# Performance work log

Hardware: AMD Instinct MI355X
Metric: run time of the kernel (lower is better)

Reference implementation:

```python
import jax, jax.numpy as jnp
import numpy as np

NUM_EMBEDDINGS = 512
EMBEDDING_DIM = 64
COMMITMENT_COST = 0.25


def setup_inputs() -> dict:
    key = jax.random.key(0)
    k1, k2 = jax.random.split(key)
    x = jax.random.normal(k1, (32, 64, 64, 64), dtype=jnp.float32)  # [B, C=D, H, W]
    # torch init: uniform(-1/K, 1/K)
    w = jax.random.uniform(k2, (NUM_EMBEDDINGS, EMBEDDING_DIM), dtype=jnp.float32,
                           minval=-1.0 / NUM_EMBEDDINGS, maxval=1.0 / NUM_EMBEDDINGS)
    return {"x": x, "w": w}


def reference(x, w):
    # [B, C, H, W] -> [B, H, W, C]
    xt = jnp.transpose(x, (0, 2, 3, 1))
    flat = xt.reshape(-1, EMBEDDING_DIM)  # [N, D]
    # squared L2 distances to each codebook vector: [N, K]
    distances = (jnp.sum(flat * flat, axis=1, keepdims=True)
                 + jnp.sum(w * w, axis=1)
                 - 2.0 * flat @ w.T)
    idx = jnp.argmin(distances, axis=1)  # [N]
    encodings = jax.nn.one_hot(idx, NUM_EMBEDDINGS, dtype=x.dtype)  # [N, K]
    quantized = w[idx].reshape(xt.shape)  # gather == one_hot @ w
    e_latent_loss = jnp.mean((jax.lax.stop_gradient(quantized) - xt) ** 2)
    q_latent_loss = jnp.mean((quantized - jax.lax.stop_gradient(xt)) ** 2)
    quant_loss = q_latent_loss + COMMITMENT_COST * e_latent_loss
    # straight-through estimator
    quantized_st = xt + jax.lax.stop_gradient(quantized - xt)
    quantized_out = jnp.transpose(quantized_st, (0, 3, 1, 2))  # back to [B, C, H, W]
    avg_probs = jnp.mean(encodings, axis=0)
    perplexity = jnp.exp(-jnp.sum(avg_probs * jnp.log(avg_probs + 1e-10)))
    return quantized_out, quant_loss, encodings, perplexity
```

## Files before the change

### kernel.cpp

```cpp
#include <hip/hip_runtime.h>
#include <math.h>

#define TB        256
#define POSB      256
#define NPOS      131072
#define KCODES    512
#define DIM       64
#define HW        4096
#define LOSS_OFF  8388608ull
#define ENC_OFF   8388609ull
#define PERP_OFF  75497473ull
#define TILE_DW   (POSB * KCODES)
#define NF4       ((TILE_DW - 4) / 4)
#define TAU       2.0e-4f

typedef __attribute__((ext_vector_type(8))) short bf16x8;
typedef __attribute__((ext_vector_type(4))) float f32x4;

__device__ __forceinline__ float tree8(float r0, float r1, float r2, float r3,
                                       float r4, float r5, float r6, float r7) {
    return __fadd_rn(__fadd_rn(__fadd_rn(r0, r1), __fadd_rn(r2, r3)),
                     __fadd_rn(__fadd_rn(r4, r5), __fadd_rn(r6, r7)));
}

extern "C" __global__ __launch_bounds__(512)
void vq_prep(const float* __restrict__ w, float* __restrict__ ww,
             int* __restrict__ counts, float* __restrict__ lossAcc,
             unsigned short* __restrict__ wfrag)
{
    const int t = threadIdx.x;
    if (blockIdx.x < 32) {
        const int ct = blockIdx.x;
        if (t < 256) {
            const int part = t >> 7, q = (t >> 6) & 1, lf = t & 63;
            const int n = lf & 15, k = ct * 16 + n;
            const float* wk = w + (size_t)k * DIM;
            unsigned short v8[8];
            #pragma unroll
            for (int j8 = 0; j8 < 8; ++j8) {
                const int d = q * 32 + ((lf >> 4) << 3) + j8;
                float v = wk[d];
                unsigned int hb = __float_as_uint(v) & 0xFFFF0000u;
                if (part == 0) {
                    v8[j8] = (unsigned short)(hb >> 16);
                } else {
                    float rr = v - __uint_as_float(hb);
                    v8[j8] = (unsigned short)(__float_as_uint(rr) >> 16);
                }
            }
            bf16x8* dst = reinterpret_cast<bf16x8*>(wfrag);
            dst[((part * 32 + ct) * 2 + q) * 64 + lf] =
                *reinterpret_cast<const bf16x8*>(v8);
        }
    } else {
        const int k = t;
        const float* wk = w + (size_t)k * DIM;
        float r[8];
        #pragma unroll
        for (int i = 0; i < 8; ++i) {
            #pragma unroll
            for (int j = 0; j < 8; ++j) {
                float v = wk[i * 8 + j];
                float pp = __fmul_rn(v, v);
                r[j] = (i == 0) ? pp : __fadd_rn(r[j], pp);
            }
        }
        ww[k] = tree8(r[0], r[1], r[2], r[3], r[4], r[5], r[6], r[7]);
        counts[k] = 0;
        if (k == 0) *lossAcc = 0.0f;
    }
}

#define FRAG(PART, CT, Q) wf[((((PART) * 32 + (CT)) * 2 + (Q)) * 64) + l]

#define TILE6(PT, B0, B1, B2, B3, WWK)                                        \
    acc = (f32x4){(WWK), (WWK), (WWK), (WWK)};                                \
    acc = __builtin_amdgcn_mfma_f32_16x16x32_bf16(aL0[PT], B0, acc, 0, 0, 0); \
    acc = __builtin_amdgcn_mfma_f32_16x16x32_bf16(aH0[PT], B2, acc, 0, 0, 0); \
    acc = __builtin_amdgcn_mfma_f32_16x16x32_bf16(aH0[PT], B0, acc, 0, 0, 0); \
    acc = __builtin_amdgcn_mfma_f32_16x16x32_bf16(aL1[PT], B1, acc, 0, 0, 0); \
    acc = __builtin_amdgcn_mfma_f32_16x16x32_bf16(aH1[PT], B3, acc, 0, 0, 0); \
    acc = __builtin_amdgcn_mfma_f32_16x16x32_bf16(aH1[PT], B1, acc, 0, 0, 0);

extern "C" __global__ __launch_bounds__(TB)
__attribute__((amdgpu_waves_per_eu(2, 8)))
void vq_main(const float* __restrict__ x, const float* __restrict__ w,
             const float* __restrict__ ww, float* __restrict__ out,
             int* __restrict__ counts, float* __restrict__ lossAcc,
             const unsigned short* __restrict__ wfrag)
{
    __shared__ __align__(16) float xtile[DIM][POSB + 1];
    __shared__ float wwlds[KCODES];
    __shared__ int   hcount[KCODES];
    __shared__ int   ccount[POSB];
    __shared__ int   clist[POSB * 4];
    __shared__ int   bestkL[POSB];

    const int tid = threadIdx.x;
    const int l   = tid & 63;
    const int wv  = tid >> 6;
    const int n0  = blockIdx.x * POSB;
    const int b   = n0 >> 12;
    const int hw0 = n0 & 4095;

    hcount[tid]      = 0;
    hcount[tid + TB] = 0;
    ccount[tid]      = 0;
    wwlds[tid]       = ww[tid];
    wwlds[tid + TB]  = ww[tid + TB];

    const float* xb = x + ((size_t)b * DIM) * HW + hw0;
    #pragma unroll
    for (int it = 0; it < 64; ++it) {
        const int idx = it * TB + tid;
        const int d = idx >> 8, ps = idx & 255;
        xtile[d][ps] = xb[(size_t)d * HW + ps];
    }
    __syncthreads();

    bf16x8 aH0[4], aH1[4], aL0[4], aL1[4];
    #pragma unroll
    for (int pt = 0; pt < 4; ++pt) {
        const int arow = (wv * 4 + pt) * 16 + (l & 15);
        #pragma unroll
        for (int q = 0; q < 2; ++q) {
            #pragma unroll
            for (int j8 = 0; j8 < 8; ++j8) {
                const int d = q * 32 + ((l >> 4) << 3) + j8;
                float v = xtile[d][arow];
                float m2 = -(v + v);
                unsigned int hb = __float_as_uint(m2) & 0xFFFF0000u;
                float rr = m2 - __uint_as_float(hb);
                short hs = (short)(hb >> 16);
                short ls = (short)(__float_as_uint(rr) >> 16);
                if (q == 0) { aH0[pt][j8] = hs; aL0[pt][j8] = ls; }
                else        { aH1[pt][j8] = hs; aL1[pt][j8] = ls; }
            }
        }
    }

    const bf16x8* wf = reinterpret_cast<const bf16x8*>(wfrag);
    const int rloc = (l >> 4) << 2;

    const size_t T0 = ENC_OFF + (size_t)blockIdx.x * TILE_DW;
    float4* zs4 = reinterpret_cast<float4*>(out + T0 + 3);
    const float4 zero4 = make_float4(0.0f, 0.0f, 0.0f, 0.0f);
    if (tid < 3)  out[T0 + tid] = 0.0f;
    if (tid == 3) out[T0 + (TILE_DW - 1)] = 0.0f;

    float rmin[4][4];
    #pragma unroll
    for (int pt = 0; pt < 4; ++pt)
        #pragma unroll
        for (int i = 0; i < 4; ++i) rmin[pt][i] = INFINITY;
    {
        bf16x8 c0 = FRAG(0, 0, 0), c1 = FRAG(0, 0, 1);
        bf16x8 c2 = FRAG(1, 0, 0), c3 = FRAG(1, 0, 1);
        float wa = wwlds[(l & 15)];
        f32x4 acc;
        #pragma unroll 1
        for (int ct = 0; ct < 32; ++ct) {
            const int nt = (ct + 1) & 31;
            bf16x8 p0 = FRAG(0, nt, 0), p1 = FRAG(0, nt, 1);
            bf16x8 p2 = FRAG(1, nt, 0), p3 = FRAG(1, nt, 1);
            float wb = wwlds[nt * 16 + (l & 15)];
            #pragma unroll
            for (int pt = 0; pt < 4; ++pt) {
                TILE6(pt, c0, c1, c2, c3, wa)
                #pragma unroll
                for (int i = 0; i < 4; ++i)
                    rmin[pt][i] = fminf(rmin[pt][i], acc[i]);
            }
            {
                const int mb = ct * (TB * 2) + tid;
                zs4[mb]              = zero4;
                zs4[mb + TB]         = zero4;
                const int mb2 = (TB * 64) + ct * (TB * 2) + tid;
                zs4[mb2]             = zero4;
                zs4[mb2 + TB]        = zero4;
            }
            c0 = p0; c1 = p1; c2 = p2; c3 = p3; wa = wb;
        }
    }
    float thr[4][4];
    #pragma unroll
    for (int pt = 0; pt < 4; ++pt) {
        #pragma unroll
        for (int mm = 1; mm < 16; mm <<= 1)
            #pragma unroll
            for (int i = 0; i < 4; ++i)
                rmin[pt][i] = fminf(rmin[pt][i], __shfl_xor(rmin[pt][i], mm));
        #pragma unroll
        for (int i = 0; i < 4; ++i) thr[pt][i] = rmin[pt][i] + TAU;
    }

    {
        bf16x8 c0 = FRAG(0, 0, 0), c1 = FRAG(0, 0, 1);
        bf16x8 c2 = FRAG(1, 0, 0), c3 = FRAG(1, 0, 1);
        float wa = wwlds[(l & 15)];
        f32x4 acc;
        #pragma unroll 1
        for (int ct = 0; ct < 32; ++ct) {
            const int nt = (ct + 1) & 31;
            bf16x8 p0 = FRAG(0, nt, 0), p1 = FRAG(0, nt, 1);
            bf16x8 p2 = FRAG(1, nt, 0), p3 = FRAG(1, nt, 1);
            float wb = wwlds[nt * 16 + (l & 15)];
            #pragma unroll
            for (int pt = 0; pt < 4; ++pt) {
                TILE6(pt, c0, c1, c2, c3, wa)
                const int prow = (wv * 4 + pt) * 16 + rloc;
                #pragma unroll
                for (int i = 0; i < 4; ++i) {
                    if (acc[i] <= thr[pt][i]) {
                        int s = atomicAdd(&ccount[prow + i], 1);
                        if (s < 4) clist[(prow + i) * 4 + s] = ct * 16 + (l & 15);
                    }
                }
            }
            {
                const int mb = 16384 + ct * (TB * 2) + tid;
                zs4[mb]       = zero4;
                if (mb + TB < NF4) zs4[mb + TB] = zero4;
                const int mb2 = 16384 + (TB * 64) + ct * (TB * 2) + tid;
                if (mb2 < NF4)      zs4[mb2]      = zero4;
                if (mb2 + TB < NF4) zs4[mb2 + TB] = zero4;
            }
            c0 = p0; c1 = p1; c2 = p2; c3 = p3; wa = wb;
        }
    }

    __syncthreads();

    {
        const int p = wv * 64 + l;
        const int cnt = ccount[p];
        int bk;
        if (cnt == 1) {
            bk = clist[p * 4 + 0];
        } else {
            float x2c[DIM];
            float r[8];
            #pragma unroll
            for (int d = 0; d < DIM; ++d) {
                float v = xtile[d][p];
                x2c[d] = v + v;
                float pp = __fmul_rn(v, v);
                r[d & 7] = (d < 8) ? pp : __fadd_rn(r[d & 7], pp);
            }
            const float A = tree8(r[0], r[1], r[2], r[3], r[4], r[5], r[6], r[7]);
            if (cnt <= 4) {
                float bd = INFINITY; int bk2 = KCODES;
                for (int c = 0; c < cnt; ++c) {
                    const int k = clist[p * 4 + c];
                    const float* wk = w + (size_t)k * DIM;
                    float s[8];
                    #pragma unroll
                    for (int i = 0; i < 8; ++i) {
                        #pragma unroll
                        for (int j = 0; j < 8; ++j) {
                            const int d = i * 8 + j;
                            float wvv = wk[d];
                            if (i == 0) s[j] = __fmul_rn(x2c[d], wvv);
                            else        s[j] = __fmaf_rn(x2c[d], wvv, s[j]);
                        }
                    }
                    float dot  = tree8(s[0], s[1], s[2], s[3], s[4], s[5], s[6], s[7]);
                    float dist = __fadd_rn(__fadd_rn(A, wwlds[k]), -dot);
                    if (dist < bd || (dist == bd && k < bk2)) { bd = dist; bk2 = k; }
                }
                bk = bk2;
            } else {
                float bd = INFINITY; int bk2 = 0;
                #pragma unroll 1
                for (int k = 0; k < KCODES; ++k) {
                    const float* wk = w + (size_t)k * DIM;
                    float s[8];
                    #pragma unroll
                    for (int i = 0; i < 8; ++i) {
                        #pragma unroll
                        for (int j = 0; j < 8; ++j) {
                            const int d = i * 8 + j;
                            float wvv = wk[d];
                            if (i == 0) s[j] = __fmul_rn(x2c[d], wvv);
                            else        s[j] = __fmaf_rn(x2c[d], wvv, s[j]);
                        }
                    }
                    float dot  = tree8(s[0], s[1], s[2], s[3], s[4], s[5], s[6], s[7]);
                    float dist = __fadd_rn(__fadd_rn(A, wwlds[k]), -dot);
                    if (dist < bd) { bd = dist; bk2 = k; }
                }
                bk = bk2;
            }
        }
        bestkL[p] = bk;
        out[ENC_OFF + (size_t)(n0 + p) * KCODES + bk] = 1.0f;
        atomicAdd(&hcount[bk], 1);
    }

    __syncthreads();

    {
        const int sp = tid;
        const int bk = bestkL[sp];
        const float4* wr = reinterpret_cast<const float4*>(w + (size_t)bk * DIM);
        float* qo = out + ((size_t)b * DIM) * HW + (hw0 + sp);
        float sse = 0.0f;
        #pragma unroll
        for (int c = 0; c < 16; ++c) {
            float4 qv = wr[c];
            const int ch = c * 4;
            qo[(size_t)(ch + 0) * HW] = qv.x;
            qo[(size_t)(ch + 1) * HW] = qv.y;
            qo[(size_t)(ch + 2) * HW] = qv.z;
            qo[(size_t)(ch + 3) * HW] = qv.w;
            float e0 = qv.x - xtile[ch + 0][sp]; sse = __fmaf_rn(e0, e0, sse);
            float e1 = qv.y - xtile[ch + 1][sp]; sse = __fmaf_rn(e1, e1, sse);
            float e2 = qv.z - xtile[ch + 2][sp]; sse = __fmaf_rn(e2, e2, sse);
            float e3 = qv.w - xtile[ch + 3][sp]; sse = __fmaf_rn(e3, e3, sse);
        }
        #pragma unroll
        for (int off = 32; off > 0; off >>= 1) sse += __shfl_down(sse, off);
        if (l == 0) atomicAdd(lossAcc, sse);
    }

    __syncthreads();

    {
        int c0 = hcount[tid];       if (c0) atomicAdd(&counts[tid], c0);
        int c1 = hcount[tid + TB];  if (c1) atomicAdd(&counts[tid + TB], c1);
    }
}

extern "C" __global__ __launch_bounds__(512)
void vq_finalize(const int* __restrict__ counts, const float* __restrict__ lossAcc,
                 float* __restrict__ out)
{
    __shared__ double sred[KCODES];
    const int t = threadIdx.x;
    double p = (double)counts[t] * (1.0 / (double)NPOS);
    sred[t] = -p * log(p + 1e-10);
    __syncthreads();
    for (int s = KCODES / 2; s > 0; s >>= 1) {
        if (t < s) sred[t] += sred[t + s];
        __syncthreads();
    }
    if (t == 0) {
        out[PERP_OFF] = (float)exp(sred[0]);
        out[LOSS_OFF] = 1.25f * (lossAcc[0] / 8388608.0f);
    }
}

extern "C" void kernel_launch(void* const* d_in, const int* in_sizes, int n_in,
                              void* d_out, int out_size, void* d_ws, size_t ws_size,
                              hipStream_t stream)
{
    const float* x = (const float*)d_in[0];
    const float* w = (const float*)d_in[1];
    float* out = (float*)d_out;

    float* ww              = (float*)d_ws;
    int*   counts          = (int*)((char*)d_ws + 2048);
    float* lossAcc         = (float*)((char*)d_ws + 4096);
    unsigned short* wfrag  = (unsigned short*)((char*)d_ws + 8192);

    vq_prep<<<33, 512, 0, stream>>>(w, ww, counts, lossAcc, wfrag);
    vq_main<<<NPOS / POSB, TB, 0, stream>>>(x, w, ww, out, counts,
                                            lossAcc, wfrag);
    vq_finalize<<<1, 512, 0, stream>>>(counts, lossAcc, out);
}
```

Before: 392.4 us.

## Fold finalize into main kernel, use nontemporal stores, deepen fragment prefetch

The change does three separate things. It removes the separate finalize launch: a global done-counter lets the last block to finish compute perplexity and the loss scale, reusing the xtile LDS as scratch. The large zero-fill of the one-hot encoding output now uses nontemporal stores so it does not pollute the caches. Codebook fragment prefetch in both MFMA passes goes from one tile ahead to two, which adds register pressure in exchange for hiding more load latency.

```diff
diff --git a/kernel.cpp b/kernel.cpp
--- a/kernel.cpp
+++ b/kernel.cpp
@@ -13,6 +13,7 @@
 #define TILE_DW   (POSB * KCODES)
 #define NF4       ((TILE_DW - 4) / 4)
 #define TAU       2.0e-4f
+#define NBLK      (NPOS / POSB)
 
 typedef __attribute__((ext_vector_type(8))) short bf16x8;
 typedef __attribute__((ext_vector_type(4))) float f32x4;
@@ -26,7 +27,7 @@
 extern "C" __global__ __launch_bounds__(512)
 void vq_prep(const float* __restrict__ w, float* __restrict__ ww,
              int* __restrict__ counts, float* __restrict__ lossAcc,
-             unsigned short* __restrict__ wfrag)
+             unsigned short* __restrict__ wfrag, int* __restrict__ donecnt)
 {
     const int t = threadIdx.x;
     if (blockIdx.x < 32) {
@@ -67,7 +68,7 @@
         }
         ww[k] = tree8(r[0], r[1], r[2], r[3], r[4], r[5], r[6], r[7]);
         counts[k] = 0;
-        if (k == 0) *lossAcc = 0.0f;
+        if (k == 0) { *lossAcc = 0.0f; *donecnt = 0; }
     }
 }
 
@@ -87,7 +88,7 @@
 void vq_main(const float* __restrict__ x, const float* __restrict__ w,
              const float* __restrict__ ww, float* __restrict__ out,
              int* __restrict__ counts, float* __restrict__ lossAcc,
-             const unsigned short* __restrict__ wfrag)
+             const unsigned short* __restrict__ wfrag, int* __restrict__ donecnt)
 {
     __shared__ __align__(16) float xtile[DIM][POSB + 1];
     __shared__ float wwlds[KCODES];
@@ -95,6 +96,7 @@
     __shared__ int   ccount[POSB];
     __shared__ int   clist[POSB * 4];
     __shared__ int   bestkL[POSB];
+    __shared__ int   lastFlag;
 
     const int tid = threadIdx.x;
     const int l   = tid & 63;
@@ -143,8 +145,8 @@
     const int rloc = (l >> 4) << 2;
 
     const size_t T0 = ENC_OFF + (size_t)blockIdx.x * TILE_DW;
-    float4* zs4 = reinterpret_cast<float4*>(out + T0 + 3);
-    const float4 zero4 = make_float4(0.0f, 0.0f, 0.0f, 0.0f);
+    f32x4* zs4 = reinterpret_cast<f32x4*>(out + T0 + 3);
+    const f32x4 zero4 = (f32x4){0.0f, 0.0f, 0.0f, 0.0f};
     if (tid < 3)  out[T0 + tid] = 0.0f;
     if (tid == 3) out[T0 + (TILE_DW - 1)] = 0.0f;
 
@@ -156,14 +158,17 @@
     {
         bf16x8 c0 = FRAG(0, 0, 0), c1 = FRAG(0, 0, 1);
         bf16x8 c2 = FRAG(1, 0, 0), c3 = FRAG(1, 0, 1);
+        bf16x8 d0 = FRAG(0, 1, 0), d1 = FRAG(0, 1, 1);
+        bf16x8 d2 = FRAG(1, 1, 0), d3 = FRAG(1, 1, 1);
         float wa = wwlds[(l & 15)];
+        float wbn = wwlds[16 + (l & 15)];
         f32x4 acc;
         #pragma unroll 1
         for (int ct = 0; ct < 32; ++ct) {
-            const int nt = (ct + 1) & 31;
-            bf16x8 p0 = FRAG(0, nt, 0), p1 = FRAG(0, nt, 1);
-            bf16x8 p2 = FRAG(1, nt, 0), p3 = FRAG(1, nt, 1);
-            float wb = wwlds[nt * 16 + (l & 15)];
+            const int ft = (ct + 2) & 31;
+            bf16x8 e0 = FRAG(0, ft, 0), e1 = FRAG(0, ft, 1);
+            bf16x8 e2 = FRAG(1, ft, 0), e3 = FRAG(1, ft, 1);
+            float wc = wwlds[ft * 16 + (l & 15)];
             #pragma unroll
             for (int pt = 0; pt < 4; ++pt) {
                 TILE6(pt, c0, c1, c2, c3, wa)
@@ -173,13 +178,14 @@
             }
             {
                 const int mb = ct * (TB * 2) + tid;
-                zs4[mb]              = zero4;
-                zs4[mb + TB]         = zero4;
+                __builtin_nontemporal_store(zero4, &zs4[mb]);
+                __builtin_nontemporal_store(zero4, &zs4[mb + TB]);
                 const int mb2 = (TB * 64) + ct * (TB * 2) + tid;
-                zs4[mb2]             = zero4;
-                zs4[mb2 + TB]        = zero4;
-            }
-            c0 = p0; c1 = p1; c2 = p2; c3 = p3; wa = wb;
+                __builtin_nontemporal_store(zero4, &zs4[mb2]);
+                __builtin_nontemporal_store(zero4, &zs4[mb2 + TB]);
+            }
+            c0 = d0; c1 = d1; c2 = d2; c3 = d3; wa = wbn;
+            d0 = e0; d1 = e1; d2 = e2; d3 = e3; wbn = wc;
         }
     }
     float thr[4][4];
@@ -197,14 +203,17 @@
     {
         bf16x8 c0 = FRAG(0, 0, 0), c1 = FRAG(0, 0, 1);
         bf16x8 c2 = FRAG(1, 0, 0), c3 = FRAG(1, 0, 1);
+        bf16x8 d0 = FRAG(0, 1, 0), d1 = FRAG(0, 1, 1);
+        bf16x8 d2 = FRAG(1, 1, 0), d3 = FRAG(1, 1, 1);
         float wa = wwlds[(l & 15)];
+        float wbn = wwlds[16 + (l & 15)];
         f32x4 acc;
         #pragma unroll 1
         for (int ct = 0; ct < 32; ++ct) {
-            const int nt = (ct + 1) & 31;
-            bf16x8 p0 = FRAG(0, nt, 0), p1 = FRAG(0, nt, 1);
-            bf16x8 p2 = FRAG(1, nt, 0), p3 = FRAG(1, nt, 1);
-            float wb = wwlds[nt * 16 + (l & 15)];
+            const int ft = (ct + 2) & 31;
+            bf16x8 e0 = FRAG(0, ft, 0), e1 = FRAG(0, ft, 1);
+            bf16x8 e2 = FRAG(1, ft, 0), e3 = FRAG(1, ft, 1);
+            float wc = wwlds[ft * 16 + (l & 15)];
             #pragma unroll
             for (int pt = 0; pt < 4; ++pt) {
                 TILE6(pt, c0, c1, c2, c3, wa)
@@ -219,13 +228,17 @@
             }
             {
                 const int mb = 16384 + ct * (TB * 2) + tid;
-                zs4[mb]       = zero4;
-                if (mb + TB < NF4) zs4[mb + TB] = zero4;
+                __builtin_nontemporal_store(zero4, &zs4[mb]);
+                if (mb + TB < NF4)
+                    __builtin_nontemporal_store(zero4, &zs4[mb + TB]);
                 const int mb2 = 16384 + (TB * 64) + ct * (TB * 2) + tid;
-                if (mb2 < NF4)      zs4[mb2]      = zero4;
-                if (mb2 + TB < NF4) zs4[mb2 + TB] = zero4;
-            }
-            c0 = p0; c1 = p1; c2 = p2; c3 = p3; wa = wb;
+                if (mb2 < NF4)
+                    __builtin_nontemporal_store(zero4, &zs4[mb2]);
+                if (mb2 + TB < NF4)
+                    __builtin_nontemporal_store(zero4, &zs4[mb2 + TB]);
+            }
+            c0 = d0; c1 = d1; c2 = d2; c3 = d3; wa = wbn;
+            d0 = e0; d1 = e1; d2 = e2; d3 = e3; wbn = wc;
         }
     }
 
@@ -329,24 +342,32 @@
         int c0 = hcount[tid];       if (c0) atomicAdd(&counts[tid], c0);
         int c1 = hcount[tid + TB];  if (c1) atomicAdd(&counts[tid + TB], c1);
     }
-}
-
-extern "C" __global__ __launch_bounds__(512)
-void vq_finalize(const int* __restrict__ counts, const float* __restrict__ lossAcc,
-                 float* __restrict__ out)
-{
-    __shared__ double sred[KCODES];
-    const int t = threadIdx.x;
-    double p = (double)counts[t] * (1.0 / (double)NPOS);
-    sred[t] = -p * log(p + 1e-10);
-    __syncthreads();
-    for (int s = KCODES / 2; s > 0; s >>= 1) {
-        if (t < s) sred[t] += sred[t + s];
+    __syncthreads();
+
+    __threadfence();
+    if (tid == 0)
+        lastFlag = (atomicAdd(donecnt, 1) == NBLK - 1) ? 1 : 0;
+    __syncthreads();
+    if (lastFlag) {
+        __threadfence();
+        double* sred = reinterpret_cast<double*>(&xtile[0][0]);
+        #pragma unroll
+        for (int u = 0; u < 2; ++u) {
+            const int k = u * TB + tid;
+            int cv = atomicAdd(&counts[k], 0);
+            double p = (double)cv * (1.0 / (double)NPOS);
+            sred[k] = -p * log(p + 1e-10);
+        }
         __syncthreads();
-    }
-    if (t == 0) {
-        out[PERP_OFF] = (float)exp(sred[0]);
-        out[LOSS_OFF] = 1.25f * (lossAcc[0] / 8388608.0f);
+        for (int s = KCODES / 2; s > 0; s >>= 1) {
+            if (tid < s) sred[tid] += sred[tid + s];
+            __syncthreads();
+        }
+        if (tid == 0) {
+            float lossv = atomicAdd(lossAcc, 0.0f);
+            out[PERP_OFF] = (float)exp(sred[0]);
+            out[LOSS_OFF] = 1.25f * (lossv / 8388608.0f);
+        }
     }
 }
 
@@ -361,10 +382,10 @@
     float* ww              = (float*)d_ws;
     int*   counts          = (int*)((char*)d_ws + 2048);
     float* lossAcc         = (float*)((char*)d_ws + 4096);
+    int*   donecnt         = (int*)((char*)d_ws + 4104);
     unsigned short* wfrag  = (unsigned short*)((char*)d_ws + 8192);
 
-    vq_prep<<<33, 512, 0, stream>>>(w, ww, counts, lossAcc, wfrag);
-    vq_main<<<NPOS / POSB, TB, 0, stream>>>(x, w, ww, out, counts,
-                                            lossAcc, wfrag);
-    vq_finalize<<<1, 512, 0, stream>>>(counts, lossAcc, out);
+    vq_prep<<<33, 512, 0, stream>>>(w, ww, counts, lossAcc, wfrag, donecnt);
+    vq_main<<<NBLK, TB, 0, stream>>>(x, w, ww, out, counts,
+                                     lossAcc, wfrag, donecnt);
 }
```

Result: slower. 483.1 us (+23.1%).
